# Kernel tuning notes

Measured on AMD Instinct MI355X. Metric: run time of the kernel, lower is better.

Reference implementation:

```python
import jax, jax.numpy as jnp
import numpy as np

N_NODES = 50000
N_EDGES = 400000
NFEAT, NHID, NOUT, NCLASS = 512, 256, 256, 8


def _glorot(key, shape):
    lim = float(np.sqrt(6.0 / (shape[0] + shape[1])))
    return jax.random.uniform(key, shape, jnp.float32, -lim, lim)


def setup_inputs() -> dict:
    key = jax.random.key(0)
    ks = jax.random.split(key, 8)
    x = jax.random.normal(ks[0], (N_NODES, NFEAT), jnp.float32)
    edge_index = jax.random.randint(ks[1], (2, N_EDGES), 0, N_NODES, jnp.int32)
    # learnable edge weight logits (init 1 - eps in the module; trained => generic values)
    edge_w_params = jnp.ones((N_EDGES,), jnp.float32) * 0.9999
    W1 = _glorot(ks[2], (NFEAT, NHID)); b1 = jnp.zeros((NHID,), jnp.float32)
    W2 = _glorot(ks[3], (NHID, NHID)); b2 = jnp.zeros((NHID,), jnp.float32)
    W3 = _glorot(ks[4], (NHID, NOUT)); b3 = jnp.zeros((NOUT,), jnp.float32)
    Wlin = _glorot(ks[5], (NHID + NHID + NOUT, NCLASS))
    blin = jnp.zeros((NCLASS,), jnp.float32)
    return {"x": x, "edge_index": edge_index, "edge_w_params": edge_w_params,
            "W1": W1, "b1": b1, "W2": W2, "b2": b2, "W3": W3, "b3": b3,
            "Wlin": Wlin, "blin": blin}


def _gcn_conv(x, W, b, src, dst, ew, n):
    """PyG GCNConv with add_self_loops=True.
    Self-loop weight is 1 (fill_value). norm = d^-1/2[src] * w * d^-1/2[dst].
    Self-loop contribution handled analytically (no edge concat).
    """
    deg = jax.ops.segment_sum(ew, dst, num_segments=n) + 1.0  # +1 self-loop weight
    dinv = jnp.where(deg > 0, jax.lax.rsqrt(deg), 0.0)
    norm = dinv[src] * ew * dinv[dst]                          # [E]
    h = x @ W                                                  # [n, out]
    agg = jax.ops.segment_sum(h[src] * norm[:, None], dst, num_segments=n)
    agg = agg + h * (dinv * dinv)[:, None]                     # self loops
    return agg + b


def reference(x, edge_index, edge_w_params, W1, b1, W2, b2, W3, b3, Wlin, blin):
    n = x.shape[0]
    src, dst = edge_index[0], edge_index[1]
    ew = jax.nn.sigmoid(edge_w_params)
    ones_ew = jnp.ones_like(ew)
    x1 = jax.nn.relu(_gcn_conv(x, W1, b1, src, dst, ew, n))    # dropout: eval mode (identity)
    x2 = jax.nn.relu(_gcn_conv(x1, W2, b2, src, dst, ew, n))
    x3 = _gcn_conv(x2, W3, b3, src, dst, ones_ew, n)           # gc3 called without edge_weight
    logits = jnp.concatenate((x1, x2, x3), axis=1) @ Wlin + blin
    return jax.nn.log_softmax(logits, axis=1)
```

## Files before the change

### kernel.cpp

```cpp
#include <hip/hip_runtime.h>
#include <math.h>

#define N_NODES 50000
#define N_EDGES 400000
#define M_PAD 50048
#define NFEAT 512
#define NHID 256
#define NCLASS 8
#define SCAN_BLOCKS ((N_NODES + 255) / 256)

typedef unsigned short u16;
typedef __attribute__((ext_vector_type(8))) unsigned short u16x8;
typedef __attribute__((ext_vector_type(8))) short s16x8;
typedef __attribute__((ext_vector_type(4))) float f32x4;

__device__ __forceinline__ float bf2f(u16 u) {
    union { unsigned int i; float f; } v; v.i = ((unsigned int)u) << 16; return v.f;
}
__device__ __forceinline__ float bf2f_hi(unsigned int packed) {
    union { unsigned int i; float f; } v; v.i = packed & 0xffff0000u; return v.f;
}
__device__ __forceinline__ float bf2f_lo(unsigned int packed) {
    union { unsigned int i; float f; } v; v.i = packed << 16; return v.f;
}
__device__ __forceinline__ u16 f2bf(float f) {
    union { float f; unsigned int i; } v; v.f = f;
    unsigned int r = v.i + 0x7fffu + ((v.i >> 16) & 1u);
    return (u16)(r >> 16);
}


__global__ void init_k(float* deg, int* cnt, int* cur) {
    int i = blockIdx.x * blockDim.x + threadIdx.x;
    if (i < N_NODES) { deg[i] = 1.0f; cnt[i] = 0; cur[i] = 0; }
}

__global__ void edge_deg_k(const float* __restrict__ p, const int* __restrict__ dst,
                           float* __restrict__ deg, int* __restrict__ cnt,
                           float* __restrict__ ew_out) {
    int e = blockIdx.x * blockDim.x + threadIdx.x;
    if (e >= N_EDGES) return;
    float ew = 1.0f / (1.0f + expf(-p[e]));
    ew_out[e] = ew;
    int d = dst[e];
    atomicAdd(&deg[d], ew);
    atomicAdd(&cnt[d], 1);
}

__global__ void finalize_dinv_k(float* __restrict__ deg, const int* __restrict__ cnt,
                                float* __restrict__ dinv3) {
    int i = blockIdx.x * blockDim.x + threadIdx.x;
    if (i < N_NODES) {
        deg[i]   = 1.0f / sqrtf(deg[i]);
        dinv3[i] = 1.0f / sqrtf(1.0f + (float)cnt[i]);
    }
}

__global__ __launch_bounds__(256) void scan1_k(const int* __restrict__ cnt,
                                               int* __restrict__ row_start,
                                               int* __restrict__ bsum) {
    __shared__ int tmp[256];
    int t = threadIdx.x;
    int g = blockIdx.x * 256 + t;
    int v = (g < N_NODES) ? cnt[g] : 0;
    tmp[t] = v;
    __syncthreads();
    #pragma unroll
    for (int off = 1; off < 256; off <<= 1) {
        int u = (t >= off) ? tmp[t - off] : 0;
        __syncthreads();
        tmp[t] += u;
        __syncthreads();
    }
    if (g < N_NODES) row_start[g] = tmp[t] - v;
    if (t == 255) bsum[blockIdx.x] = tmp[255];
}

__global__ __launch_bounds__(256) void scan2_k(int* __restrict__ bsum) {
    __shared__ int tmp[256];
    int t = threadIdx.x;
    int v = (t < SCAN_BLOCKS) ? bsum[t] : 0;
    tmp[t] = v;
    __syncthreads();
    #pragma unroll
    for (int off = 1; off < 256; off <<= 1) {
        int u = (t >= off) ? tmp[t - off] : 0;
        __syncthreads();
        tmp[t] += u;
        __syncthreads();
    }
    if (t < SCAN_BLOCKS) bsum[t] = tmp[t] - v;
}

__global__ __launch_bounds__(256) void scan3_k(int* __restrict__ row_start,
                                               const int* __restrict__ bsum) {
    int t = threadIdx.x;
    int g = blockIdx.x * 256 + t;
    if (g < N_NODES) row_start[g] += bsum[blockIdx.x];
    if (g == 0) row_start[N_NODES] = N_EDGES;
}

__global__ void fill_k(const int* __restrict__ src, const int* __restrict__ dst,
                       const float* __restrict__ ew, const float* __restrict__ dinv,
                       const float* __restrict__ dinv3,
                       const int* __restrict__ row_start, int* __restrict__ cur,
                       uint2* __restrict__ ep, uint2* __restrict__ ep3) {
    int e = blockIdx.x * blockDim.x + threadIdx.x;
    if (e >= N_EDGES) return;
    int s = src[e], d = dst[e];
    float w  = dinv[s] * ew[e] * dinv[d];
    float w3 = dinv3[s] * dinv3[d];
    int p = atomicAdd(&cur[d], 1);
    int slot = row_start[d] + p;
    ep[slot]  = make_uint2((unsigned int)s, __float_as_uint(w));
    ep3[slot] = make_uint2((unsigned int)s, __float_as_uint(w3));
}


__global__ void wtrans_all_k(const float* __restrict__ W1, const float* __restrict__ W2,
                             const float* __restrict__ W3, u16* __restrict__ wt1,
                             u16* __restrict__ wt2, u16* __restrict__ wt3) {
    int idx = blockIdx.x * 256 + threadIdx.x;
    const float* W; u16* Wt; int K;
    if (idx < 256 * 512)           { W = W1; Wt = wt1; K = 512; }
    else if (idx < 256 * 512 + 256 * 256) { idx -= 256 * 512; W = W2; Wt = wt2; K = 256; }
    else if (idx < 256 * 512 + 2 * 256 * 256) { idx -= 256 * 512 + 256 * 256; W = W3; Wt = wt3; K = 256; }
    else return;
    int n = idx / K, k = idx - n * K;
    Wt[(size_t)n * K + k] = f2bf(W[(size_t)k * 256 + n]);
}

__global__ void zeropad_k(u16* a, u16* b) {
    int i = blockIdx.x * 256 + threadIdx.x;
    if (i < (M_PAD - N_NODES) * 256) {
        a[(size_t)N_NODES * 256 + i] = 0;
        b[(size_t)N_NODES * 256 + i] = 0;
    }
}


__device__ __forceinline__ u16x8 ldcvt_f32(const float* p, bool ok) {
    u16x8 o = {0, 0, 0, 0, 0, 0, 0, 0};
    if (ok) {
        float4 a = *(const float4*)p;
        float4 b = *(const float4*)(p + 4);
        o[0] = f2bf(a.x); o[1] = f2bf(a.y); o[2] = f2bf(a.z); o[3] = f2bf(a.w);
        o[4] = f2bf(b.x); o[5] = f2bf(b.y); o[6] = f2bf(b.z); o[7] = f2bf(b.w);
    }
    return o;
}

template <bool AF32>
__global__ __launch_bounds__(256) void gemm_bf16_k(const void* __restrict__ Ap,
                                                   const u16* __restrict__ BT,
                                                   u16* __restrict__ C, int K) {
    __shared__ u16 Asl[128 * 40];
    __shared__ u16 Bsl[128 * 40];
    int tid = threadIdx.x;
    int lane = tid & 63;
    int wid = tid >> 6;
    int wm = wid >> 1, wn = wid & 1;
    int row0 = blockIdx.x * 128;
    int col0 = blockIdx.y * 128;

    int c0 = tid, c1 = tid + 256;
    int ar0 = c0 >> 2, ak0 = (c0 & 3) << 3;
    int ar1 = c1 >> 2, ak1 = (c1 & 3) << 3;
    const u16*   A16 = (const u16*)Ap;
    const float* A32 = (const float*)Ap;
    bool ok0 = (row0 + ar0) < N_NODES;
    bool ok1 = (row0 + ar1) < N_NODES;
    const u16* Ag0 = A16 + (size_t)(row0 + ar0) * K + ak0;
    const u16* Ag1 = A16 + (size_t)(row0 + ar1) * K + ak1;
    const float* Af0 = A32 + (size_t)(row0 + ar0) * K + ak0;
    const float* Af1 = A32 + (size_t)(row0 + ar1) * K + ak1;
    const u16* Bg0 = BT + (size_t)(col0 + ar0) * K + ak0;
    const u16* Bg1 = BT + (size_t)(col0 + ar1) * K + ak1;
    int la0 = ar0 * 40 + ak0, la1 = ar1 * 40 + ak1;

    u16x8 ra0, ra1;
    if (AF32) { ra0 = ldcvt_f32(Af0, ok0); ra1 = ldcvt_f32(Af1, ok1); }
    else      { ra0 = *(const u16x8*)Ag0;  ra1 = *(const u16x8*)Ag1; }
    u16x8 rb0 = *(const u16x8*)Bg0;
    u16x8 rb1 = *(const u16x8*)Bg1;

    f32x4 acc[4][4] = {};

    int arow = wm * 64 + (lane & 15);
    int bcol = wn * 64 + (lane & 15);
    int kg = (lane >> 4) << 3;

    int nt = K >> 5;
    for (int t = 0; t < nt; ++t) {
        __syncthreads();
        *(u16x8*)&Asl[la0] = ra0; *(u16x8*)&Asl[la1] = ra1;
        *(u16x8*)&Bsl[la0] = rb0; *(u16x8*)&Bsl[la1] = rb1;
        __syncthreads();
        if (t + 1 < nt) {
            int ko = (t + 1) << 5;
            if (AF32) { ra0 = ldcvt_f32(Af0 + ko, ok0); ra1 = ldcvt_f32(Af1 + ko, ok1); }
            else      { ra0 = *(const u16x8*)(Ag0 + ko); ra1 = *(const u16x8*)(Ag1 + ko); }
            rb0 = *(const u16x8*)(Bg0 + ko);
            rb1 = *(const u16x8*)(Bg1 + ko);
        }
        s16x8 af[4], bf[4];
        #pragma unroll
        for (int m = 0; m < 4; ++m)
            af[m] = *(const s16x8*)&Asl[(arow + m * 16) * 40 + kg];
        #pragma unroll
        for (int n = 0; n < 4; ++n)
            bf[n] = *(const s16x8*)&Bsl[(bcol + n * 16) * 40 + kg];
        #pragma unroll
        for (int m = 0; m < 4; ++m)
            #pragma unroll
            for (int n = 0; n < 4; ++n)
                acc[m][n] = __builtin_amdgcn_mfma_f32_16x16x32_bf16(af[m], bf[n], acc[m][n], 0, 0, 0);
    }

    int crow0 = row0 + wm * 64 + ((lane >> 4) << 2);
    int ccol  = col0 + wn * 64 + (lane & 15);
    #pragma unroll
    for (int m = 0; m < 4; ++m)
        #pragma unroll
        for (int n = 0; n < 4; ++n)
            #pragma unroll
            for (int r = 0; r < 4; ++r)
                C[(size_t)(crow0 + m * 16 + r) * 256 + ccol + n * 16] = f2bf(acc[m][n][r]);
}


template <bool RELU>
__global__ __launch_bounds__(256) void gather_k(const u16* __restrict__ h,
                                                const int* __restrict__ row_start,
                                                const uint2* __restrict__ ep,
                                                const float* __restrict__ dinv,
                                                const float* __restrict__ bias,
                                                u16* __restrict__ outb) {
    int node = blockIdx.x * 4 + (threadIdx.x >> 6);
    if (node >= N_NODES) return;
    int lane = threadIdx.x & 63;

    float di = dinv[node];
    float sw = di * di;
    uint2 hv = *(const uint2*)(h + (size_t)node * 256 + lane * 4);
    float4 acc;
    acc.x = bf2f_lo(hv.x) * sw; acc.y = bf2f_hi(hv.x) * sw;
    acc.z = bf2f_lo(hv.y) * sw; acc.w = bf2f_hi(hv.y) * sw;

    int beg = row_start[node], end = row_start[node + 1];
    int j = beg;
    for (; j + 4 <= end; j += 4) {
        uint2 e0 = ep[j], e1 = ep[j + 1], e2 = ep[j + 2], e3 = ep[j + 3];
        uint2 u0 = *(const uint2*)(h + (size_t)e0.x * 256 + lane * 4);
        uint2 u1 = *(const uint2*)(h + (size_t)e1.x * 256 + lane * 4);
        uint2 u2 = *(const uint2*)(h + (size_t)e2.x * 256 + lane * 4);
        uint2 u3 = *(const uint2*)(h + (size_t)e3.x * 256 + lane * 4);
        float w0 = __uint_as_float(e0.y), w1 = __uint_as_float(e1.y);
        float w2 = __uint_as_float(e2.y), w3 = __uint_as_float(e3.y);
        acc.x += bf2f_lo(u0.x) * w0; acc.y += bf2f_hi(u0.x) * w0;
        acc.z += bf2f_lo(u0.y) * w0; acc.w += bf2f_hi(u0.y) * w0;
        acc.x += bf2f_lo(u1.x) * w1; acc.y += bf2f_hi(u1.x) * w1;
        acc.z += bf2f_lo(u1.y) * w1; acc.w += bf2f_hi(u1.y) * w1;
        acc.x += bf2f_lo(u2.x) * w2; acc.y += bf2f_hi(u2.x) * w2;
        acc.z += bf2f_lo(u2.y) * w2; acc.w += bf2f_hi(u2.y) * w2;
        acc.x += bf2f_lo(u3.x) * w3; acc.y += bf2f_hi(u3.x) * w3;
        acc.z += bf2f_lo(u3.y) * w3; acc.w += bf2f_hi(u3.y) * w3;
    }
    for (; j < end; ++j) {
        uint2 e = ep[j];
        float w = __uint_as_float(e.y);
        uint2 uv = *(const uint2*)(h + (size_t)e.x * 256 + lane * 4);
        acc.x += bf2f_lo(uv.x) * w; acc.y += bf2f_hi(uv.x) * w;
        acc.z += bf2f_lo(uv.y) * w; acc.w += bf2f_hi(uv.y) * w;
    }
    float4 bv = ((const float4*)bias)[lane];
    acc.x += bv.x; acc.y += bv.y; acc.z += bv.z; acc.w += bv.w;
    if (RELU) {
        acc.x = fmaxf(acc.x, 0.f); acc.y = fmaxf(acc.y, 0.f);
        acc.z = fmaxf(acc.z, 0.f); acc.w = fmaxf(acc.w, 0.f);
    }
    uint2 o;
    o.x = (unsigned int)f2bf(acc.x) | ((unsigned int)f2bf(acc.y) << 16);
    o.y = (unsigned int)f2bf(acc.z) | ((unsigned int)f2bf(acc.w) << 16);
    *(uint2*)(outb + (size_t)node * 256 + lane * 4) = o;
}


template <bool FIRST>
__global__ __launch_bounds__(256) void logits_acc_k(const u16* __restrict__ x,
                                                    const float* __restrict__ Wlin,
                                                    const float* __restrict__ blin,
                                                    float* __restrict__ logits, int seg) {
    __shared__ float Ws[256 * 8];
    int tid = threadIdx.x;
    const float* Wseg = Wlin + (size_t)seg * 256 * 8;
    for (int i = tid; i < 2048; i += 256) Ws[i] = Wseg[i];
    __syncthreads();
    int row = blockIdx.x * 32 + (tid >> 3);
    int c = tid & 7;
    if (row >= N_NODES) return;
    const u16* xr = x + (size_t)row * 256;
    float acc = 0.f;
    for (int k8 = 0; k8 < 32; ++k8) {
        u16x8 v = *(const u16x8*)&xr[k8 * 8];
        #pragma unroll
        for (int i = 0; i < 8; ++i) acc += bf2f(v[i]) * Ws[(k8 * 8 + i) * 8 + c];
    }
    float* lp = &logits[(size_t)row * 8 + c];
    if (FIRST) *lp = acc + blin[c];
    else       *lp += acc;
}

__global__ void log_softmax_k(const float* __restrict__ logits, float* __restrict__ out) {
    int row = blockIdx.x * blockDim.x + threadIdx.x;
    if (row >= N_NODES) return;
    float4 a = *(const float4*)&logits[(size_t)row * 8];
    float4 b = *(const float4*)&logits[(size_t)row * 8 + 4];
    float m = fmaxf(fmaxf(fmaxf(a.x, a.y), fmaxf(a.z, a.w)),
                    fmaxf(fmaxf(b.x, b.y), fmaxf(b.z, b.w)));
    float s = expf(a.x - m) + expf(a.y - m) + expf(a.z - m) + expf(a.w - m)
            + expf(b.x - m) + expf(b.y - m) + expf(b.z - m) + expf(b.w - m);
    float ls = logf(s) + m;
    float* o = &out[(size_t)row * 8];
    o[0] = a.x - ls; o[1] = a.y - ls; o[2] = a.z - ls; o[3] = a.w - ls;
    o[4] = b.x - ls; o[5] = b.y - ls; o[6] = b.z - ls; o[7] = b.w - ls;
}


extern "C" void kernel_launch(void* const* d_in, const int* in_sizes, int n_in,
                              void* d_out, int out_size, void* d_ws, size_t ws_size,
                              hipStream_t stream) {
    const float* x    = (const float*)d_in[0];
    const int*   ei   = (const int*)d_in[1];
    const float* ewp  = (const float*)d_in[2];
    const float* W1   = (const float*)d_in[3];
    const float* b1   = (const float*)d_in[4];
    const float* W2   = (const float*)d_in[5];
    const float* b2   = (const float*)d_in[6];
    const float* W3   = (const float*)d_in[7];
    const float* b3   = (const float*)d_in[8];
    const float* Wlin = (const float*)d_in[9];
    const float* blin = (const float*)d_in[10];
    float* out = (float*)d_out;

    const int* src = ei;
    const int* dst = ei + N_EDGES;

    float* ws = (float*)d_ws;
    float* ew     = ws;
    float* dinv   = ew + N_EDGES;
    float* dinv3  = dinv + N_NODES;
    float* logits = dinv3 + N_NODES;
    int* cnt       = (int*)(logits + (size_t)N_NODES * 8);
    int* cur       = cnt + N_NODES;
    int* row_start = cur + N_NODES;
    int* bsum      = row_start + N_NODES + 1;
    uint2* ep  = (uint2*)(((uintptr_t)(bsum + SCAN_BLOCKS) + 127) & ~(uintptr_t)127);
    uint2* ep3 = ep + N_EDGES;
    u16* hb  = (u16*)(ep3 + N_EDGES);
    u16* x1b = hb  + (size_t)M_PAD * 256;
    u16* x2b = x1b + (size_t)M_PAD * 256;
    u16* x3b = x2b + (size_t)M_PAD * 256;
    u16* wt1 = x3b + (size_t)M_PAD * 256;
    u16* wt2 = wt1 + 256 * 512;
    u16* wt3 = wt2 + 256 * 256;

    dim3 blk(256);
    int nodeBlocks  = (N_NODES + 255) / 256;
    int edgeBlocks  = (N_EDGES + 255) / 256;
    int gathBlocks  = (N_NODES + 3) / 4;
    int rowBlocks32 = (N_NODES + 31) / 32;
    dim3 gemmGrid(M_PAD / 128, 2);

    init_k<<<nodeBlocks, blk, 0, stream>>>(dinv, cnt, cur);
    edge_deg_k<<<edgeBlocks, blk, 0, stream>>>(ewp, dst, dinv, cnt, ew);
    finalize_dinv_k<<<nodeBlocks, blk, 0, stream>>>(dinv, cnt, dinv3);
    scan1_k<<<SCAN_BLOCKS, blk, 0, stream>>>(cnt, row_start, bsum);
    scan2_k<<<1, blk, 0, stream>>>(bsum);
    scan3_k<<<SCAN_BLOCKS, blk, 0, stream>>>(row_start, bsum);
    fill_k<<<edgeBlocks, blk, 0, stream>>>(src, dst, ew, dinv, dinv3, row_start, cur, ep, ep3);

    wtrans_all_k<<<(256 * 512 + 2 * 256 * 256 + 255) / 256, blk, 0, stream>>>(
        W1, W2, W3, wt1, wt2, wt3);
    zeropad_k<<<48, blk, 0, stream>>>(x1b, x2b);

    gemm_bf16_k<true><<<gemmGrid, blk, 0, stream>>>(x, wt1, hb, NFEAT);
    gather_k<true><<<gathBlocks, blk, 0, stream>>>(hb, row_start, ep, dinv, b1, x1b);
    logits_acc_k<true><<<rowBlocks32, blk, 0, stream>>>(x1b, Wlin, blin, logits, 0);

    gemm_bf16_k<false><<<gemmGrid, blk, 0, stream>>>(x1b, wt2, hb, NHID);
    gather_k<true><<<gathBlocks, blk, 0, stream>>>(hb, row_start, ep, dinv, b2, x2b);
    logits_acc_k<false><<<rowBlocks32, blk, 0, stream>>>(x2b, Wlin, blin, logits, 1);

    gemm_bf16_k<false><<<gemmGrid, blk, 0, stream>>>(x2b, wt3, hb, NHID);
    gather_k<false><<<gathBlocks, blk, 0, stream>>>(hb, row_start, ep3, dinv3, b3, x3b);
    logits_acc_k<false><<<rowBlocks32, blk, 0, stream>>>(x3b, Wlin, blin, logits, 2);

    log_softmax_k<<<nodeBlocks, blk, 0, stream>>>(logits, out);
}
```

Before: 319.1 us.

## Use direct global-to-LDS loads and 64-wide K tiles in bf16 GEMM

```diff
diff --git a/kernel.cpp b/kernel.cpp
--- a/kernel.cpp
+++ b/kernel.cpp
@@ -27,6 +27,12 @@
     union { float f; unsigned int i; } v; v.f = f;
     unsigned int r = v.i + 0x7fffu + ((v.i >> 16) & 1u);
     return (u16)(r >> 16);
+}
+
+__device__ __forceinline__ void gload16(const void* g, void* l) {
+    __builtin_amdgcn_global_load_lds(
+        (const __attribute__((address_space(1))) void*)g,
+        (__attribute__((address_space(3))) void*)l, 16, 0, 0);
 }
 
 
@@ -154,8 +160,8 @@
 __global__ __launch_bounds__(256) void gemm_bf16_k(const void* __restrict__ Ap,
                                                    const u16* __restrict__ BT,
                                                    u16* __restrict__ C, int K) {
-    __shared__ u16 Asl[128 * 40];
-    __shared__ u16 Bsl[128 * 40];
+    __shared__ u16 Asl[128 * 64];
+    __shared__ u16 Bsl[128 * 64];
     int tid = threadIdx.x;
     int lane = tid & 63;
     int wid = tid >> 6;
@@ -163,58 +169,61 @@
     int row0 = blockIdx.x * 128;
     int col0 = blockIdx.y * 128;
 
-    int c0 = tid, c1 = tid + 256;
-    int ar0 = c0 >> 2, ak0 = (c0 & 3) << 3;
-    int ar1 = c1 >> 2, ak1 = (c1 & 3) << 3;
     const u16*   A16 = (const u16*)Ap;
     const float* A32 = (const float*)Ap;
-    bool ok0 = (row0 + ar0) < N_NODES;
-    bool ok1 = (row0 + ar1) < N_NODES;
-    const u16* Ag0 = A16 + (size_t)(row0 + ar0) * K + ak0;
-    const u16* Ag1 = A16 + (size_t)(row0 + ar1) * K + ak1;
-    const float* Af0 = A32 + (size_t)(row0 + ar0) * K + ak0;
-    const float* Af1 = A32 + (size_t)(row0 + ar1) * K + ak1;
-    const u16* Bg0 = BT + (size_t)(col0 + ar0) * K + ak0;
-    const u16* Bg1 = BT + (size_t)(col0 + ar1) * K + ak1;
-    int la0 = ar0 * 40 + ak0, la1 = ar1 * 40 + ak1;
-
-    u16x8 ra0, ra1;
-    if (AF32) { ra0 = ldcvt_f32(Af0, ok0); ra1 = ldcvt_f32(Af1, ok1); }
-    else      { ra0 = *(const u16x8*)Ag0;  ra1 = *(const u16x8*)Ag1; }
-    u16x8 rb0 = *(const u16x8*)Bg0;
-    u16x8 rb1 = *(const u16x8*)Bg1;
+
+    int srow = lane >> 3, sc = lane & 7;
 
     f32x4 acc[4][4] = {};
-
     int arow = wm * 64 + (lane & 15);
     int bcol = wn * 64 + (lane & 15);
-    int kg = (lane >> 4) << 3;
-
-    int nt = K >> 5;
+
+    int nt = K >> 6;
     for (int t = 0; t < nt; ++t) {
         __syncthreads();
-        *(u16x8*)&Asl[la0] = ra0; *(u16x8*)&Asl[la1] = ra1;
-        *(u16x8*)&Bsl[la0] = rb0; *(u16x8*)&Bsl[la1] = rb1;
-        __syncthreads();
-        if (t + 1 < nt) {
-            int ko = (t + 1) << 5;
-            if (AF32) { ra0 = ldcvt_f32(Af0 + ko, ok0); ra1 = ldcvt_f32(Af1 + ko, ok1); }
-            else      { ra0 = *(const u16x8*)(Ag0 + ko); ra1 = *(const u16x8*)(Ag1 + ko); }
-            rb0 = *(const u16x8*)(Bg0 + ko);
-            rb1 = *(const u16x8*)(Bg1 + ko);
+        if constexpr (AF32) {
+            #pragma unroll
+            for (int i = 0; i < 4; ++i) {
+                int chunk = i * 256 + tid;
+                int r = chunk >> 3, c = chunk & 7;
+                int gr = row0 + r;
+                u16x8 v = ldcvt_f32(A32 + (size_t)gr * K + t * 64 + c * 8, gr < N_NODES);
+                *(u16x8*)&Asl[r * 64 + c * 8] = v;
+            }
+        } else {
+            #pragma unroll
+            for (int i = 0; i < 4; ++i) {
+                int base = i * 4 + wid;
+                int r = base * 8 + srow;
+                gload16(A16 + (size_t)(row0 + r) * K + t * 64 + sc * 8,
+                        &Asl[base * 512]);
+            }
         }
-        s16x8 af[4], bf[4];
         #pragma unroll
-        for (int m = 0; m < 4; ++m)
-            af[m] = *(const s16x8*)&Asl[(arow + m * 16) * 40 + kg];
+        for (int i = 0; i < 4; ++i) {
+            int base = i * 4 + wid;
+            int r = base * 8 + srow;
+            gload16(BT + (size_t)(col0 + r) * K + t * 64 + sc * 8,
+                    &Bsl[base * 512]);
+        }
+        __syncthreads();
+
         #pragma unroll
-        for (int n = 0; n < 4; ++n)
-            bf[n] = *(const s16x8*)&Bsl[(bcol + n * 16) * 40 + kg];
-        #pragma unroll
-        for (int m = 0; m < 4; ++m)
+        for (int h = 0; h < 2; ++h) {
+            int kg = ((lane >> 4) << 3) + h * 32;
+            s16x8 af[4], bf[4];
+            #pragma unroll
+            for (int m = 0; m < 4; ++m)
+                af[m] = *(const s16x8*)&Asl[(arow + m * 16) * 64 + kg];
             #pragma unroll
             for (int n = 0; n < 4; ++n)
-                acc[m][n] = __builtin_amdgcn_mfma_f32_16x16x32_bf16(af[m], bf[n], acc[m][n], 0, 0, 0);
+                bf[n] = *(const s16x8*)&Bsl[(bcol + n * 16) * 64 + kg];
+            #pragma unroll
+            for (int m = 0; m < 4; ++m)
+                #pragma unroll
+                for (int n = 0; n < 4; ++n)
+                    acc[m][n] = __builtin_amdgcn_mfma_f32_16x16x32_bf16(af[m], bf[n], acc[m][n], 0, 0, 0);
+        }
     }
 
     int crow0 = row0 + wm * 64 + ((lane >> 4) << 2);
```

Result: slower. 326.7 us (+2.4%).

## Replace LDS-tiled GEMM with single-wave register-direct MFMA kernel

Applied to the files above, without the earlier changes.

```diff
diff --git a/kernel.cpp b/kernel.cpp
--- a/kernel.cpp
+++ b/kernel.cpp
@@ -151,78 +151,50 @@
 }
 
 template <bool AF32>
-__global__ __launch_bounds__(256) void gemm_bf16_k(const void* __restrict__ Ap,
+__global__ __launch_bounds__(64, 2) void gemm_rr_k(const void* __restrict__ Ap,
                                                    const u16* __restrict__ BT,
                                                    u16* __restrict__ C, int K) {
-    __shared__ u16 Asl[128 * 40];
-    __shared__ u16 Bsl[128 * 40];
-    int tid = threadIdx.x;
-    int lane = tid & 63;
-    int wid = tid >> 6;
-    int wm = wid >> 1, wn = wid & 1;
-    int row0 = blockIdx.x * 128;
-    int col0 = blockIdx.y * 128;
-
-    int c0 = tid, c1 = tid + 256;
-    int ar0 = c0 >> 2, ak0 = (c0 & 3) << 3;
-    int ar1 = c1 >> 2, ak1 = (c1 & 3) << 3;
+    int lane = threadIdx.x;
+    int row0 = blockIdx.y * 64;
+    int col0 = blockIdx.x * 128;
     const u16*   A16 = (const u16*)Ap;
     const float* A32 = (const float*)Ap;
-    bool ok0 = (row0 + ar0) < N_NODES;
-    bool ok1 = (row0 + ar1) < N_NODES;
-    const u16* Ag0 = A16 + (size_t)(row0 + ar0) * K + ak0;
-    const u16* Ag1 = A16 + (size_t)(row0 + ar1) * K + ak1;
-    const float* Af0 = A32 + (size_t)(row0 + ar0) * K + ak0;
-    const float* Af1 = A32 + (size_t)(row0 + ar1) * K + ak1;
-    const u16* Bg0 = BT + (size_t)(col0 + ar0) * K + ak0;
-    const u16* Bg1 = BT + (size_t)(col0 + ar1) * K + ak1;
-    int la0 = ar0 * 40 + ak0, la1 = ar1 * 40 + ak1;
-
-    u16x8 ra0, ra1;
-    if (AF32) { ra0 = ldcvt_f32(Af0, ok0); ra1 = ldcvt_f32(Af1, ok1); }
-    else      { ra0 = *(const u16x8*)Ag0;  ra1 = *(const u16x8*)Ag1; }
-    u16x8 rb0 = *(const u16x8*)Bg0;
-    u16x8 rb1 = *(const u16x8*)Bg1;
-
-    f32x4 acc[4][4] = {};
-
-    int arow = wm * 64 + (lane & 15);
-    int bcol = wn * 64 + (lane & 15);
-    int kg = (lane >> 4) << 3;
+
+    int fr = lane & 15;
+    int kb = (lane >> 4) << 3;
+
+    f32x4 acc[4][8] = {};
 
     int nt = K >> 5;
     for (int t = 0; t < nt; ++t) {
-        __syncthreads();
-        *(u16x8*)&Asl[la0] = ra0; *(u16x8*)&Asl[la1] = ra1;
-        *(u16x8*)&Bsl[la0] = rb0; *(u16x8*)&Bsl[la1] = rb1;
-        __syncthreads();
-        if (t + 1 < nt) {
-            int ko = (t + 1) << 5;
-            if (AF32) { ra0 = ldcvt_f32(Af0 + ko, ok0); ra1 = ldcvt_f32(Af1 + ko, ok1); }
-            else      { ra0 = *(const u16x8*)(Ag0 + ko); ra1 = *(const u16x8*)(Ag1 + ko); }
-            rb0 = *(const u16x8*)(Bg0 + ko);
-            rb1 = *(const u16x8*)(Bg1 + ko);
+        int k0 = t * 32 + kb;
+        s16x8 af[4];
+        #pragma unroll
+        for (int m = 0; m < 4; ++m) {
+            int gr = row0 + m * 16 + fr;
+            if constexpr (AF32) {
+                af[m] = (s16x8)ldcvt_f32(A32 + (size_t)gr * K + k0, gr < N_NODES);
+            } else {
+                af[m] = *(const s16x8*)(A16 + (size_t)gr * K + k0);
+            }
         }
-        s16x8 af[4], bf[4];
-        #pragma unroll
-        for (int m = 0; m < 4; ++m)
-            af[m] = *(const s16x8*)&Asl[(arow + m * 16) * 40 + kg];
-        #pragma unroll
-        for (int n = 0; n < 4; ++n)
-            bf[n] = *(const s16x8*)&Bsl[(bcol + n * 16) * 40 + kg];
+        s16x8 bf[8];
+        #pragma unroll
+        for (int n = 0; n < 8; ++n)
+            bf[n] = *(const s16x8*)(BT + (size_t)(col0 + n * 16 + fr) * K + k0);
         #pragma unroll
         for (int m = 0; m < 4; ++m)
             #pragma unroll
-            for (int n = 0; n < 4; ++n)
+            for (int n = 0; n < 8; ++n)
                 acc[m][n] = __builtin_amdgcn_mfma_f32_16x16x32_bf16(af[m], bf[n], acc[m][n], 0, 0, 0);
     }
 
-    int crow0 = row0 + wm * 64 + ((lane >> 4) << 2);
-    int ccol  = col0 + wn * 64 + (lane & 15);
+    int crow0 = row0 + ((lane >> 4) << 2);
+    int ccol  = col0 + fr;
     #pragma unroll
     for (int m = 0; m < 4; ++m)
         #pragma unroll
-        for (int n = 0; n < 4; ++n)
+        for (int n = 0; n < 8; ++n)
             #pragma unroll
             for (int r = 0; r < 4; ++r)
                 C[(size_t)(crow0 + m * 16 + r) * 256 + ccol + n * 16] = f2bf(acc[m][n][r]);
@@ -366,11 +338,12 @@
     u16* wt3 = wt2 + 256 * 256;
 
     dim3 blk(256);
+    dim3 blk64(64);
     int nodeBlocks  = (N_NODES + 255) / 256;
     int edgeBlocks  = (N_EDGES + 255) / 256;
     int gathBlocks  = (N_NODES + 3) / 4;
     int rowBlocks32 = (N_NODES + 31) / 32;
-    dim3 gemmGrid(M_PAD / 128, 2);
+    dim3 gemmGrid(2, M_PAD / 64);
 
     init_k<<<nodeBlocks, blk, 0, stream>>>(dinv, cnt, cur);
     edge_deg_k<<<edgeBlocks, blk, 0, stream>>>(ewp, dst, dinv, cnt, ew);
@@ -384,15 +357,15 @@
         W1, W2, W3, wt1, wt2, wt3);
     zeropad_k<<<48, blk, 0, stream>>>(x1b, x2b);
 
-    gemm_bf16_k<true><<<gemmGrid, blk, 0, stream>>>(x, wt1, hb, NFEAT);
+    gemm_rr_k<true><<<gemmGrid, blk64, 0, stream>>>(x, wt1, hb, NFEAT);
     gather_k<true><<<gathBlocks, blk, 0, stream>>>(hb, row_start, ep, dinv, b1, x1b);
     logits_acc_k<true><<<rowBlocks32, blk, 0, stream>>>(x1b, Wlin, blin, logits, 0);
 
-    gemm_bf16_k<false><<<gemmGrid, blk, 0, stream>>>(x1b, wt2, hb, NHID);
+    gemm_rr_k<false><<<gemmGrid, blk64, 0, stream>>>(x1b, wt2, hb, NHID);
     gather_k<true><<<gathBlocks, blk, 0, stream>>>(hb, row_start, ep, dinv, b2, x2b);
     logits_acc_k<false><<<rowBlocks32, blk, 0, stream>>>(x2b, Wlin, blin, logits, 1);
 
-    gemm_bf16_k<false><<<gemmGrid, blk, 0, stream>>>(x2b, wt3, hb, NHID);
+    gemm_rr_k<false><<<gemmGrid, blk64, 0, stream>>>(x2b, wt3, hb, NHID);
     gather_k<false><<<gathBlocks, blk, 0, stream>>>(hb, row_start, ep3, dinv3, b3, x3b);
     logits_acc_k<false><<<rowBlocks32, blk, 0, stream>>>(x3b, Wlin, blin, logits, 2);
 
```

New measurement: 343.8 us. +7.7%, slower.

## Double-buffer GEMM shared tiles and split gather edges across half-waves

Applied to the files above, without the earlier changes.

```diff
diff --git a/kernel.cpp b/kernel.cpp
--- a/kernel.cpp
+++ b/kernel.cpp
@@ -154,8 +154,8 @@
 __global__ __launch_bounds__(256) void gemm_bf16_k(const void* __restrict__ Ap,
                                                    const u16* __restrict__ BT,
                                                    u16* __restrict__ C, int K) {
-    __shared__ u16 Asl[128 * 40];
-    __shared__ u16 Bsl[128 * 40];
+    __shared__ u16 Asl[2][128 * 40];
+    __shared__ u16 Bsl[2][128 * 40];
     int tid = threadIdx.x;
     int lane = tid & 63;
     int wid = tid >> 6;
@@ -178,24 +178,23 @@
     const u16* Bg1 = BT + (size_t)(col0 + ar1) * K + ak1;
     int la0 = ar0 * 40 + ak0, la1 = ar1 * 40 + ak1;
 
-    u16x8 ra0, ra1;
+    u16x8 ra0, ra1, rb0, rb1;
     if (AF32) { ra0 = ldcvt_f32(Af0, ok0); ra1 = ldcvt_f32(Af1, ok1); }
     else      { ra0 = *(const u16x8*)Ag0;  ra1 = *(const u16x8*)Ag1; }
-    u16x8 rb0 = *(const u16x8*)Bg0;
-    u16x8 rb1 = *(const u16x8*)Bg1;
+    rb0 = *(const u16x8*)Bg0;
+    rb1 = *(const u16x8*)Bg1;
+    *(u16x8*)&Asl[0][la0] = ra0; *(u16x8*)&Asl[0][la1] = ra1;
+    *(u16x8*)&Bsl[0][la0] = rb0; *(u16x8*)&Bsl[0][la1] = rb1;
+    __syncthreads();
 
     f32x4 acc[4][4] = {};
-
     int arow = wm * 64 + (lane & 15);
     int bcol = wn * 64 + (lane & 15);
     int kg = (lane >> 4) << 3;
 
     int nt = K >> 5;
     for (int t = 0; t < nt; ++t) {
-        __syncthreads();
-        *(u16x8*)&Asl[la0] = ra0; *(u16x8*)&Asl[la1] = ra1;
-        *(u16x8*)&Bsl[la0] = rb0; *(u16x8*)&Bsl[la1] = rb1;
-        __syncthreads();
+        int cur = t & 1;
         if (t + 1 < nt) {
             int ko = (t + 1) << 5;
             if (AF32) { ra0 = ldcvt_f32(Af0 + ko, ok0); ra1 = ldcvt_f32(Af1 + ko, ok1); }
@@ -206,15 +205,20 @@
         s16x8 af[4], bf[4];
         #pragma unroll
         for (int m = 0; m < 4; ++m)
-            af[m] = *(const s16x8*)&Asl[(arow + m * 16) * 40 + kg];
+            af[m] = *(const s16x8*)&Asl[cur][(arow + m * 16) * 40 + kg];
         #pragma unroll
         for (int n = 0; n < 4; ++n)
-            bf[n] = *(const s16x8*)&Bsl[(bcol + n * 16) * 40 + kg];
+            bf[n] = *(const s16x8*)&Bsl[cur][(bcol + n * 16) * 40 + kg];
         #pragma unroll
         for (int m = 0; m < 4; ++m)
             #pragma unroll
             for (int n = 0; n < 4; ++n)
                 acc[m][n] = __builtin_amdgcn_mfma_f32_16x16x32_bf16(af[m], bf[n], acc[m][n], 0, 0, 0);
+        if (t + 1 < nt) {
+            *(u16x8*)&Asl[cur ^ 1][la0] = ra0; *(u16x8*)&Asl[cur ^ 1][la1] = ra1;
+            *(u16x8*)&Bsl[cur ^ 1][la0] = rb0; *(u16x8*)&Bsl[cur ^ 1][la1] = rb1;
+            __syncthreads();
+        }
     }
 
     int crow0 = row0 + wm * 64 + ((lane >> 4) << 2);
@@ -228,6 +232,13 @@
                 C[(size_t)(crow0 + m * 16 + r) * 256 + ccol + n * 16] = f2bf(acc[m][n][r]);
 }
 
+
+__device__ __forceinline__ void fma8(float* acc, uint4 u, float w) {
+    acc[0] += bf2f_lo(u.x) * w; acc[1] += bf2f_hi(u.x) * w;
+    acc[2] += bf2f_lo(u.y) * w; acc[3] += bf2f_hi(u.y) * w;
+    acc[4] += bf2f_lo(u.z) * w; acc[5] += bf2f_hi(u.z) * w;
+    acc[6] += bf2f_lo(u.w) * w; acc[7] += bf2f_hi(u.w) * w;
+}
 
 template <bool RELU>
 __global__ __launch_bounds__(256) void gather_k(const u16* __restrict__ h,
@@ -239,50 +250,57 @@
     int node = blockIdx.x * 4 + (threadIdx.x >> 6);
     if (node >= N_NODES) return;
     int lane = threadIdx.x & 63;
+    int half = lane >> 5;
+    int c = lane & 31;
 
     float di = dinv[node];
     float sw = di * di;
-    uint2 hv = *(const uint2*)(h + (size_t)node * 256 + lane * 4);
-    float4 acc;
-    acc.x = bf2f_lo(hv.x) * sw; acc.y = bf2f_hi(hv.x) * sw;
-    acc.z = bf2f_lo(hv.y) * sw; acc.w = bf2f_hi(hv.y) * sw;
+    uint4 hv = *(const uint4*)(h + (size_t)node * 256 + c * 8);
+    float acc[8];
+    if (half == 0) {
+        acc[0] = bf2f_lo(hv.x) * sw; acc[1] = bf2f_hi(hv.x) * sw;
+        acc[2] = bf2f_lo(hv.y) * sw; acc[3] = bf2f_hi(hv.y) * sw;
+        acc[4] = bf2f_lo(hv.z) * sw; acc[5] = bf2f_hi(hv.z) * sw;
+        acc[6] = bf2f_lo(hv.w) * sw; acc[7] = bf2f_hi(hv.w) * sw;
+    } else {
+        #pragma unroll
+        for (int i = 0; i < 8; ++i) acc[i] = 0.f;
+    }
 
     int beg = row_start[node], end = row_start[node + 1];
-    int j = beg;
-    for (; j + 4 <= end; j += 4) {
-        uint2 e0 = ep[j], e1 = ep[j + 1], e2 = ep[j + 2], e3 = ep[j + 3];
-        uint2 u0 = *(const uint2*)(h + (size_t)e0.x * 256 + lane * 4);
-        uint2 u1 = *(const uint2*)(h + (size_t)e1.x * 256 + lane * 4);
-        uint2 u2 = *(const uint2*)(h + (size_t)e2.x * 256 + lane * 4);
-        uint2 u3 = *(const uint2*)(h + (size_t)e3.x * 256 + lane * 4);
-        float w0 = __uint_as_float(e0.y), w1 = __uint_as_float(e1.y);
-        float w2 = __uint_as_float(e2.y), w3 = __uint_as_float(e3.y);
-        acc.x += bf2f_lo(u0.x) * w0; acc.y += bf2f_hi(u0.x) * w0;
-        acc.z += bf2f_lo(u0.y) * w0; acc.w += bf2f_hi(u0.y) * w0;
-        acc.x += bf2f_lo(u1.x) * w1; acc.y += bf2f_hi(u1.x) * w1;
-        acc.z += bf2f_lo(u1.y) * w1; acc.w += bf2f_hi(u1.y) * w1;
-        acc.x += bf2f_lo(u2.x) * w2; acc.y += bf2f_hi(u2.x) * w2;
-        acc.z += bf2f_lo(u2.y) * w2; acc.w += bf2f_hi(u2.y) * w2;
-        acc.x += bf2f_lo(u3.x) * w3; acc.y += bf2f_hi(u3.x) * w3;
-        acc.z += bf2f_lo(u3.y) * w3; acc.w += bf2f_hi(u3.y) * w3;
-    }
-    for (; j < end; ++j) {
-        uint2 e = ep[j];
-        float w = __uint_as_float(e.y);
-        uint2 uv = *(const uint2*)(h + (size_t)e.x * 256 + lane * 4);
-        acc.x += bf2f_lo(uv.x) * w; acc.y += bf2f_hi(uv.x) * w;
-        acc.z += bf2f_lo(uv.y) * w; acc.w += bf2f_hi(uv.y) * w;
-    }
-    float4 bv = ((const float4*)bias)[lane];
-    acc.x += bv.x; acc.y += bv.y; acc.z += bv.z; acc.w += bv.w;
-    if (RELU) {
-        acc.x = fmaxf(acc.x, 0.f); acc.y = fmaxf(acc.y, 0.f);
-        acc.z = fmaxf(acc.z, 0.f); acc.w = fmaxf(acc.w, 0.f);
-    }
-    uint2 o;
-    o.x = (unsigned int)f2bf(acc.x) | ((unsigned int)f2bf(acc.y) << 16);
-    o.y = (unsigned int)f2bf(acc.z) | ((unsigned int)f2bf(acc.w) << 16);
-    *(uint2*)(outb + (size_t)node * 256 + lane * 4) = o;
+    int jh = beg + half;
+    for (; jh + 2 < end; jh += 4) {
+        uint2 e0 = ep[jh], e1 = ep[jh + 2];
+        uint4 u0 = *(const uint4*)(h + (size_t)e0.x * 256 + c * 8);
+        uint4 u1 = *(const uint4*)(h + (size_t)e1.x * 256 + c * 8);
+        fma8(acc, u0, __uint_as_float(e0.y));
+        fma8(acc, u1, __uint_as_float(e1.y));
+    }
+    for (; jh < end; jh += 2) {
+        uint2 e = ep[jh];
+        uint4 u = *(const uint4*)(h + (size_t)e.x * 256 + c * 8);
+        fma8(acc, u, __uint_as_float(e.y));
+    }
+
+    #pragma unroll
+    for (int i = 0; i < 8; ++i) acc[i] += __shfl_xor(acc[i], 32);
+
+    if (half == 0) {
+        float4 bv0 = *(const float4*)&bias[c * 8];
+        float4 bv1 = *(const float4*)&bias[c * 8 + 4];
+        acc[0] += bv0.x; acc[1] += bv0.y; acc[2] += bv0.z; acc[3] += bv0.w;
+        acc[4] += bv1.x; acc[5] += bv1.y; acc[6] += bv1.z; acc[7] += bv1.w;
+        if (RELU) {
+            #pragma unroll
+            for (int i = 0; i < 8; ++i) acc[i] = fmaxf(acc[i], 0.f);
+        }
+        uint4 o;
+        o.x = (unsigned int)f2bf(acc[0]) | ((unsigned int)f2bf(acc[1]) << 16);
+        o.y = (unsigned int)f2bf(acc[2]) | ((unsigned int)f2bf(acc[3]) << 16);
+        o.z = (unsigned int)f2bf(acc[4]) | ((unsigned int)f2bf(acc[5]) << 16);
+        o.w = (unsigned int)f2bf(acc[6]) | ((unsigned int)f2bf(acc[7]) << 16);
+        *(uint4*)(outb + (size_t)node * 256 + c * 8) = o;
+    }
 }
 
 
```

Measured after the change: 324.6 us. Within noise of the previous version (+1.7%).
